# Optimization experiments

Hardware: AMD Instinct MI355X
Metric: run time of the kernel (lower is better)

## Reference

```python
import jax, jax.numpy as jnp
import numpy as np

EMBED_DIM = 1024
B, S = 4, 4096


def setup_inputs() -> dict:
    key = jax.random.key(0)
    kx, kq, kk, kv = jax.random.split(key, 4)
    x = jax.random.normal(kx, (B, S, EMBED_DIM), dtype=jnp.float32)
    W_Q = jax.random.normal(kq, (EMBED_DIM, EMBED_DIM), dtype=jnp.float32)
    W_K = jax.random.normal(kk, (EMBED_DIM, EMBED_DIM), dtype=jnp.float32)
    W_V = jax.random.normal(kv, (EMBED_DIM, EMBED_DIM), dtype=jnp.float32)
    return {"x": x, "W_Q": W_Q, "W_K": W_K, "W_V": W_V}


def reference(x, W_Q, W_K, W_V):
    # Q, K, V: [B, S, D]
    Q = x @ W_Q
    K = x @ W_K
    V = x @ W_V
    scale = 1.0 / jnp.sqrt(jnp.float32(EMBED_DIM))
    # scores: [B, S, S] (full score matrix, as in the original)
    scores = jnp.einsum('bsd,btd->bst', Q, K) * scale
    attn = jax.nn.softmax(scores, axis=-1)
    # output: [B, S, D]
    Z = jnp.einsum('bst,btd->bsd', attn, V)
    return Z
```

## Files before the change

kernel.cpp:

```cpp
#include <hip/hip_runtime.h>


typedef _Float16 half8 __attribute__((ext_vector_type(8)));
typedef _Float16 half4v __attribute__((ext_vector_type(4)));
typedef float floatx4 __attribute__((ext_vector_type(4)));

__device__ __forceinline__ void glds16(const _Float16* g, _Float16* l) {
    __builtin_amdgcn_global_load_lds(
        (const __attribute__((address_space(1))) void*)g,
        (__attribute__((address_space(3))) void*)l, 16, 0, 0);
}


struct QKTD { const _Float16* a; const _Float16* b; int ko; };

#define QK_VM(n) asm volatile("s_waitcnt vmcnt(" #n ")" ::: "memory")
#define QK_NOP ((void)0)

#define QK_PHASE(BUF, Q, STAGES, WAITS)                                         \
    do {                                                                        \
        if ((Q) == 0) {                                                         \
            _Pragma("unroll") for (int mi = 0; mi < 4; ++mi) {                  \
                af[mi][0] = *(const half8*)&sA[(BUF)*16384 + (abase + mi*16)*64 + s0]; \
                af[mi][1] = *(const half8*)&sA[(BUF)*16384 + (abase + mi*16)*64 + s1]; \
            }                                                                   \
        }                                                                       \
        half8 bf[2][2];                                                         \
        _Pragma("unroll") for (int nj = 0; nj < 2; ++nj) {                      \
            bf[nj][0] = *(const half8*)&sB[(BUF)*16384 + (bbase + (Q)*32 + nj*16)*64 + s0]; \
            bf[nj][1] = *(const half8*)&sB[(BUF)*16384 + (bbase + (Q)*32 + nj*16)*64 + s1]; \
        }                                                                       \
        STAGES;                                                                 \
        __builtin_amdgcn_sched_barrier(0);           \
        __builtin_amdgcn_s_barrier();                                           \
        asm volatile("s_waitcnt lgkmcnt(0)" ::: "memory");                      \
        __builtin_amdgcn_sched_barrier(0);                                      \
        __builtin_amdgcn_s_setprio(1);                                          \
        _Pragma("unroll") for (int mi = 0; mi < 4; ++mi)                        \
            _Pragma("unroll") for (int nj = 0; nj < 2; ++nj) {                  \
                acc[mi][(Q)*2 + nj] = __builtin_amdgcn_mfma_f32_16x16x32_f16(   \
                    af[mi][0], bf[nj][0], acc[mi][(Q)*2 + nj], 0, 0, 0);        \
                acc[mi][(Q)*2 + nj] = __builtin_amdgcn_mfma_f32_16x16x32_f16(   \
                    af[mi][1], bf[nj][1], acc[mi][(Q)*2 + nj], 0, 0, 0);        \
            }                                                                   \
        __builtin_amdgcn_s_setprio(0);                                          \
        WAITS;                                                                  \
        __builtin_amdgcn_s_barrier();                                           \
        __builtin_amdgcn_sched_barrier(0);                                      \
    } while (0)

__global__ __launch_bounds__(512, 2) void qk8(
    const _Float16* __restrict__ QH, const _Float16* __restrict__ QL,
    const _Float16* __restrict__ KH, const _Float16* __restrict__ KL,
    float* __restrict__ Sc, float* __restrict__ pmax, float scale)
{
    __shared__ _Float16 sA[2 * 256 * 64];
    __shared__ _Float16 sB[2 * 256 * 64];

    const int tid = threadIdx.x;
    const int bm = blockIdx.y, bn = blockIdx.x;
    const int lane = tid & 63, w = tid >> 6;
    const int quad = lane >> 4, lrow = lane & 15;
    const int wm = w >> 1, wn = w & 1;
    const int sx = lrow & 7;
    const int s0 = (quad ^ sx) * 8;
    const int s1 = s0 ^ 32;
    const int abase = wm * 64 + lrow;
    const int bbase = wn * 128 + lrow;
    const int wbase = w * 512;

    const int srow = tid >> 3;
    const int scol = ((tid & 7) ^ (srow & 7)) * 8;
    const size_t ga = (size_t)(bm * 256 + srow) * 1024 + scol;
    const size_t gb = (size_t)(bn * 256 + srow) * 1024 + scol;

    floatx4 acc[4][8] = {};
    half8 af[4][2];

    auto td = [&](int t) {
        const int d = t / 3, m = t - d * 3;
        return QKTD{m == 2 ? QL : QH, m == 1 ? KL : KH, d * 64};
    };
    auto stageA4 = [&](int b, QKTD s) {
        const _Float16* g = s.a + ga + s.ko;
        _Float16* l = sA + b * 16384 + wbase;
        glds16(g, l);
        glds16(g + 64 * 1024, l + 4096);
        glds16(g + 128 * 1024, l + 8192);
        glds16(g + 192 * 1024, l + 12288);
    };
    auto stageBq = [&](int b, int qr, QKTD s) {
        glds16(s.b + gb + (size_t)(qr * 64) * 1024 + s.ko,
               sB + b * 16384 + qr * 4096 + wbase);
    };

    {
        QKTD t0 = td(0), t1 = td(1);
        stageA4(0, t0);
        stageBq(0, 0, t0); stageBq(0, 2, t0);
        stageBq(0, 1, t0); stageBq(0, 3, t0);
        stageA4(1, t1);
        stageBq(1, 0, t1); stageBq(1, 2, t1);
    }
    __builtin_amdgcn_sched_barrier(0);
    QK_VM(6);
    __builtin_amdgcn_s_barrier();
    __builtin_amdgcn_sched_barrier(0);

    #pragma unroll 1
    for (int i = 0; i < 24; ++i) {
        const int i2 = 2 * i + 2 < 47 ? 2 * i + 2 : 47;
        const int i3 = 2 * i + 3 < 47 ? 2 * i + 3 : 47;
        const QKTD t1 = td(2 * i + 1);
        const QKTD ta = td(i2);
        const QKTD tb = td(i3);
        QK_PHASE(0, 0, { stageBq(1, 1, t1); stageBq(1, 3, t1); }, QK_NOP);
        QK_PHASE(0, 1, stageA4(0, ta), QK_VM(12));
        QK_PHASE(0, 2, { stageBq(0, 0, ta); stageBq(0, 2, ta); }, QK_NOP);
        QK_PHASE(0, 3, QK_NOP, QK_VM(8));
        QK_PHASE(1, 0, { stageBq(0, 1, ta); stageBq(0, 3, ta); }, QK_NOP);
        QK_PHASE(1, 1, stageA4(1, tb), QK_VM(12));
        QK_PHASE(1, 2, { stageBq(1, 0, tb); stageBq(1, 2, tb); }, QK_NOP);
        QK_PHASE(1, 3, QK_NOP, QK_VM(8));
    }

    QK_VM(0);
    __builtin_amdgcn_sched_barrier(0);

    #pragma unroll
    for (int mi = 0; mi < 4; ++mi) {
        #pragma unroll
        for (int r = 0; r < 4; ++r) {
            const int grow = bm * 256 + wm * 64 + mi * 16 + quad * 4 + r;
            float v[8];
            #pragma unroll
            for (int nc = 0; nc < 8; ++nc) v[nc] = acc[mi][nc][r] * scale;
            float mx = fmaxf(fmaxf(fmaxf(v[0], v[1]), fmaxf(v[2], v[3])),
                             fmaxf(fmaxf(v[4], v[5]), fmaxf(v[6], v[7])));
            #pragma unroll
            for (int off = 1; off < 16; off <<= 1)
                mx = fmaxf(mx, __shfl_xor(mx, off));
            if (lrow == 0) pmax[(size_t)grow * 32 + bn * 2 + wn] = mx;
            float* so = Sc + (size_t)grow * 4096 + bn * 256 + wn * 128;
            #pragma unroll
            for (int nc = 0; nc < 8; ++nc) so[nc * 16 + lrow] = v[nc];
        }
    }
}


template <bool SPLITIN, int OMODE, bool PMAX>
__global__ __launch_bounds__(256, 2) void gemm_nt(
    const _Float16* __restrict__ AH, const _Float16* __restrict__ AL,
    const _Float16* BH, const _Float16* BL,
    void* out0, void* out1,
    const float* __restrict__ rdiv, float* __restrict__ pmax,
    float scale, int M, int N, int K,
    const _Float16* BH2, const _Float16* BL2, void* o0b, void* o1b)
{
    if (blockIdx.z == 1) { BH = BH2; BL = BL2; out0 = o0b; out1 = o1b; }

    __shared__ _Float16 sAH[2 * 128 * 32];
    __shared__ _Float16 sBH[2 * 128 * 32];
    __shared__ _Float16 sAL[SPLITIN ? 2 * 128 * 32 : 8];
    __shared__ _Float16 sBL[SPLITIN ? 2 * 128 * 32 : 8];

    const int tid = threadIdx.x;
    const int bm = blockIdx.y, bn = blockIdx.x;
    const int lane = tid & 63, quad = lane >> 4, lrow = lane & 15;
    const int wave = tid >> 6, wm = wave >> 1, wn = wave & 1;

    const int wb = (tid & 192) * 8;
    const size_t g0 = (size_t)(tid >> 2) * K + (tid & 3) * 8;
    const size_t g1 = (size_t)((256 + tid) >> 2) * K + (tid & 3) * 8;
    const _Float16* pA0 = AH + (size_t)bm * 128 * K + g0;
    const _Float16* pA1 = AH + (size_t)bm * 128 * K + g1;
    const _Float16* pB0 = BH + (size_t)bn * 128 * K + g0;
    const _Float16* pB1 = BH + (size_t)bn * 128 * K + g1;
    const _Float16* pA0L = SPLITIN ? (AL + (size_t)bm * 128 * K + g0) : nullptr;
    const _Float16* pA1L = SPLITIN ? (AL + (size_t)bm * 128 * K + g1) : nullptr;
    const _Float16* pB0L = SPLITIN ? (BL + (size_t)bn * 128 * K + g0) : nullptr;
    const _Float16* pB1L = SPLITIN ? (BL + (size_t)bn * 128 * K + g1) : nullptr;

    floatx4 acc[4][4] = {};

    const int aoff = (wm * 64 + lrow) * 32 + quad * 8;
    const int boff = (wn * 64 + lrow) * 32 + quad * 8;

    glds16(pA0, sAH + wb);        glds16(pA1, sAH + 2048 + wb);
    glds16(pB0, sBH + wb);        glds16(pB1, sBH + 2048 + wb);
    if (SPLITIN) {
        glds16(pA0L, sAL + wb);   glds16(pA1L, sAL + 2048 + wb);
        glds16(pB0L, sBL + wb);   glds16(pB1L, sBL + 2048 + wb);
    }
    pA0 += 32; pA1 += 32; pB0 += 32; pB1 += 32;
    if (SPLITIN) { pA0L += 32; pA1L += 32; pB0L += 32; pB1L += 32; }

    int cur = 0;
    for (int k0 = 0; k0 < K; k0 += 32) {
        __syncthreads();

        if (k0 + 32 < K) {
            const int nb = (cur ^ 1) * 4096;
            glds16(pA0, sAH + nb + wb);        glds16(pA1, sAH + nb + 2048 + wb);
            glds16(pB0, sBH + nb + wb);        glds16(pB1, sBH + nb + 2048 + wb);
            if (SPLITIN) {
                glds16(pA0L, sAL + nb + wb);   glds16(pA1L, sAL + nb + 2048 + wb);
                glds16(pB0L, sBL + nb + wb);   glds16(pB1L, sBL + nb + 2048 + wb);
            }
            pA0 += 32; pA1 += 32; pB0 += 32; pB1 += 32;
            if (SPLITIN) { pA0L += 32; pA1L += 32; pB0L += 32; pB1L += 32; }
        }

        const int cb = cur * 4096;
        half8 aH[4], bH[4], aL[4], bL[4];
        #pragma unroll
        for (int i = 0; i < 4; ++i) {
            aH[i] = *(const half8*)&sAH[cb + aoff + i * 16 * 32];
            bH[i] = *(const half8*)&sBH[cb + boff + i * 16 * 32];
            if (SPLITIN) {
                aL[i] = *(const half8*)&sAL[cb + aoff + i * 16 * 32];
                bL[i] = *(const half8*)&sBL[cb + boff + i * 16 * 32];
            }
        }
        #pragma unroll
        for (int mi = 0; mi < 4; ++mi)
            #pragma unroll
            for (int nj = 0; nj < 4; ++nj) {
                acc[mi][nj] = __builtin_amdgcn_mfma_f32_16x16x32_f16(
                    aH[mi], bH[nj], acc[mi][nj], 0, 0, 0);
                if (SPLITIN) {
                    acc[mi][nj] = __builtin_amdgcn_mfma_f32_16x16x32_f16(
                        aH[mi], bL[nj], acc[mi][nj], 0, 0, 0);
                    acc[mi][nj] = __builtin_amdgcn_mfma_f32_16x16x32_f16(
                        aL[mi], bH[nj], acc[mi][nj], 0, 0, 0);
                }
            }
        cur ^= 1;
    }

    #pragma unroll
    for (int mi = 0; mi < 4; ++mi) {
        #pragma unroll
        for (int r = 0; r < 4; ++r) {
            const int grow = bm * 128 + wm * 64 + mi * 16 + quad * 4 + r;
            float s = scale;
            if (OMODE == 1) s = scale / rdiv[grow];
            float v[4];
            #pragma unroll
            for (int nj = 0; nj < 4; ++nj) v[nj] = acc[mi][nj][r] * s;
            if (PMAX) {
                float mx = fmaxf(fmaxf(v[0], v[1]), fmaxf(v[2], v[3]));
                #pragma unroll
                for (int off = 1; off < 16; off <<= 1)
                    mx = fmaxf(mx, __shfl_xor(mx, off));
                if (lrow == 0) pmax[(size_t)grow * 64 + bn * 2 + wn] = mx;
            }
            #pragma unroll
            for (int nj = 0; nj < 4; ++nj) {
                const int gcol = bn * 128 + wn * 64 + nj * 16 + lrow;
                const size_t idx = (size_t)grow * N + gcol;
                if (OMODE <= 1) {
                    ((float*)out0)[idx] = v[nj];
                } else if (OMODE == 2) {
                    ((_Float16*)out0)[idx] = (_Float16)v[nj];
                } else {
                    const _Float16 h = (_Float16)v[nj];
                    ((_Float16*)out0)[idx] = h;
                    ((_Float16*)out1)[idx] = (_Float16)(v[nj] - (float)h);
                }
            }
        }
    }
}

__global__ __launch_bounds__(256) void split_scale(
    const float* __restrict__ x, _Float16* __restrict__ hi,
    _Float16* __restrict__ lo, int n)
{
    int i = (blockIdx.x * 256 + threadIdx.x) * 4;
    const int stride = gridDim.x * 256 * 4;
    for (; i < n; i += stride) {
        float4 v = *(const float4*)(x + i);
        float a[4] = {v.x * 256.f, v.y * 256.f, v.z * 256.f, v.w * 256.f};
        half4v h, l;
        #pragma unroll
        for (int j = 0; j < 4; ++j) {
            h[j] = (_Float16)a[j];
            l[j] = (_Float16)(a[j] - (float)h[j]);
        }
        *(half4v*)(hi + i) = h;
        *(half4v*)(lo + i) = l;
    }
}

__global__ __launch_bounds__(256) void wprep3(
    const float* __restrict__ W0, const float* __restrict__ W1,
    const float* __restrict__ W2,
    _Float16* __restrict__ h0, _Float16* __restrict__ l0,
    _Float16* __restrict__ h1, _Float16* __restrict__ l1,
    _Float16* __restrict__ h2, int dim)
{
    const int z = blockIdx.z;
    const float* W = (z == 0) ? W0 : (z == 1) ? W1 : W2;
    _Float16* hiT = (z == 0) ? h0 : (z == 1) ? h1 : h2;
    _Float16* loT = (z == 0) ? l0 : (z == 1) ? l1 : nullptr;

    __shared__ float t[32][33];
    const int n0 = blockIdx.x * 32, k0 = blockIdx.y * 32;
    const int tx = threadIdx.x, ty = threadIdx.y;
    #pragma unroll
    for (int i = 0; i < 4; ++i)
        t[ty + 8 * i][tx] = 256.f * W[(size_t)(k0 + ty + 8 * i) * dim + n0 + tx];
    __syncthreads();
    #pragma unroll
    for (int i = 0; i < 4; ++i) {
        const int nn = ty + 8 * i;
        const float v = t[tx][nn];
        const _Float16 h = (_Float16)v;
        const size_t o = (size_t)(n0 + nn) * dim + k0 + tx;
        hiT[o] = h;
        if (loT) loT[o] = (_Float16)(v - (float)h);
    }
}

__global__ __launch_bounds__(256) void softmax_p(
    const float* __restrict__ Sc, const float* __restrict__ pmax,
    _Float16* __restrict__ P, float* __restrict__ rowsum)
{
    __shared__ float red[8];
    const int tid = threadIdx.x;
    const int row = blockIdx.x;
    const float* srow = Sc + (size_t)row * 4096;
    _Float16* prow = P + (size_t)row * 4096;

    if (tid < 32) {
        float m = pmax[(size_t)row * 32 + tid];
        #pragma unroll
        for (int off = 16; off; off >>= 1) m = fmaxf(m, __shfl_xor(m, off));
        if (tid == 0) red[0] = m;
    }
    __syncthreads();
    const float rmax = red[0];

    float s = 0.f;
    for (int c = tid * 4; c < 4096; c += 1024) {
        float4 v = *(const float4*)(srow + c);
        float p0 = __expf(v.x - rmax), p1 = __expf(v.y - rmax);
        float p2 = __expf(v.z - rmax), p3 = __expf(v.w - rmax);
        s += p0 + p1 + p2 + p3;
        half4v h = {(_Float16)p0, (_Float16)p1, (_Float16)p2, (_Float16)p3};
        *(half4v*)(prow + c) = h;
    }
    #pragma unroll
    for (int off = 32; off; off >>= 1) s += __shfl_xor(s, off, 64);
    if ((tid & 63) == 0) red[4 + (tid >> 6)] = s;
    __syncthreads();
    if (tid == 0) rowsum[row] = red[4] + red[5] + red[6] + red[7];
}

extern "C" void kernel_launch(void* const* d_in, const int* in_sizes, int n_in,
                              void* d_out, int out_size, void* d_ws, size_t ws_size,
                              hipStream_t stream) {
    const int Bb = 4, S = 4096, D = 1024;
    const size_t SD = (size_t)S * D;
    const size_t SS = (size_t)S * S;

    const float* x  = (const float*)d_in[0];
    const float* WQ = (const float*)d_in[1];
    const float* WK = (const float*)d_in[2];
    const float* WV = (const float*)d_in[3];
    float* out = (float*)d_out;

    char* w = (char*)d_ws;
    _Float16* WQhT = (_Float16*)w;  w += (size_t)D * D * 2;
    _Float16* WQlT = (_Float16*)w;  w += (size_t)D * D * 2;
    _Float16* WKhT = (_Float16*)w;  w += (size_t)D * D * 2;
    _Float16* WKlT = (_Float16*)w;  w += (size_t)D * D * 2;
    _Float16* WvhT = (_Float16*)w;  w += (size_t)D * D * 2;
    _Float16* xhi  = (_Float16*)w;  w += SD * 2;
    _Float16* xlo  = (_Float16*)w;  w += SD * 2;
    _Float16* Qhi  = (_Float16*)w;  w += SD * 2;
    _Float16* Qlo  = (_Float16*)w;  w += SD * 2;
    _Float16* Khi  = (_Float16*)w;  w += SD * 2;
    _Float16* Klo  = (_Float16*)w;  w += SD * 2;
    _Float16* VT   = (_Float16*)w;  w += SD * 2;
    float*    rowsum = (float*)w;   w += (size_t)S * 4;
    float*    pmax = (float*)w;     w += (size_t)S * 64 * 4;
    float*    Sc   = (float*)w;     w += SS * 4;
    _Float16* P    = (_Float16*)w;  w += SS * 2;

    const float kInv256 = 0.00390625f;
    const float kScScale = 4.76837158203125e-7f;

    dim3 blk(256);

    wprep3<<<dim3(32, 32, 3), dim3(32, 8), 0, stream>>>(
        WQ, WK, WV, WQhT, WQlT, WKhT, WKlT, WvhT, D);

    for (int b = 0; b < Bb; ++b) {
        const float* xb = x + (size_t)b * SD;
        float* outb = out + (size_t)b * SD;

        split_scale<<<dim3(4096), blk, 0, stream>>>(xb, xhi, xlo, (int)SD);

        gemm_nt<true, 3, false><<<dim3(D / 128, S / 128, 2), blk, 0, stream>>>(
            xhi, xlo, WQhT, WQlT, Qhi, Qlo, nullptr, nullptr, kInv256, S, D, D,
            WKhT, WKlT, Khi, Klo);

        gemm_nt<false, 2, false><<<dim3(S / 128, D / 128, 1), blk, 0, stream>>>(
            WvhT, nullptr, xhi, nullptr, VT, nullptr, nullptr, nullptr, kInv256,
            D, S, D, nullptr, nullptr, nullptr, nullptr);

        qk8<<<dim3(S / 256, S / 256), dim3(512), 0, stream>>>(
            Qhi, Qlo, Khi, Klo, Sc, pmax, kScScale);

        softmax_p<<<dim3(S), blk, 0, stream>>>(Sc, pmax, P, rowsum);

        gemm_nt<false, 1, false><<<dim3(D / 128, S / 128, 1), blk, 0, stream>>>(
            P, nullptr, VT, nullptr, outb, nullptr, rowsum, nullptr, kInv256,
            S, D, S, nullptr, nullptr, nullptr, nullptr);
    }
}
```

Before: 1.196 ms.

## Restructure QK GEMM pipeline to two barriers per K-tile with register double-buffered B

Replaces the eight-phase loop, which had two block barriers per quarter-tile, with a group schedule that software-pipelines LDS reads of B fragments into alternating register buffers so each MFMA batch overlaps the next fragment load. Global-to-LDS staging for a whole tile is issued at once after a single barrier, cutting the number of s_barrier syncs per tile from eight to two. This adds register pressure from the extra B fragment buffers and leaves less slack between staging and consumption.

```diff
diff --git a/kernel.cpp b/kernel.cpp
--- a/kernel.cpp
+++ b/kernel.cpp
@@ -15,38 +15,54 @@
 struct QKTD { const _Float16* a; const _Float16* b; int ko; };
 
 #define QK_VM(n) asm volatile("s_waitcnt vmcnt(" #n ")" ::: "memory")
-#define QK_NOP ((void)0)
-
-#define QK_PHASE(BUF, Q, STAGES, WAITS)                                         \
-    do {                                                                        \
-        if ((Q) == 0) {                                                         \
-            _Pragma("unroll") for (int mi = 0; mi < 4; ++mi) {                  \
-                af[mi][0] = *(const half8*)&sA[(BUF)*16384 + (abase + mi*16)*64 + s0]; \
-                af[mi][1] = *(const half8*)&sA[(BUF)*16384 + (abase + mi*16)*64 + s1]; \
-            }                                                                   \
-        }                                                                       \
-        half8 bf[2][2];                                                         \
-        _Pragma("unroll") for (int nj = 0; nj < 2; ++nj) {                      \
-            bf[nj][0] = *(const half8*)&sB[(BUF)*16384 + (bbase + (Q)*32 + nj*16)*64 + s0]; \
-            bf[nj][1] = *(const half8*)&sB[(BUF)*16384 + (bbase + (Q)*32 + nj*16)*64 + s1]; \
-        }                                                                       \
-        STAGES;                                                                 \
-        __builtin_amdgcn_sched_barrier(0);           \
-        __builtin_amdgcn_s_barrier();                                           \
-        asm volatile("s_waitcnt lgkmcnt(0)" ::: "memory");                      \
-        __builtin_amdgcn_sched_barrier(0);                                      \
-        __builtin_amdgcn_s_setprio(1);                                          \
-        _Pragma("unroll") for (int mi = 0; mi < 4; ++mi)                        \
-            _Pragma("unroll") for (int nj = 0; nj < 2; ++nj) {                  \
-                acc[mi][(Q)*2 + nj] = __builtin_amdgcn_mfma_f32_16x16x32_f16(   \
-                    af[mi][0], bf[nj][0], acc[mi][(Q)*2 + nj], 0, 0, 0);        \
-                acc[mi][(Q)*2 + nj] = __builtin_amdgcn_mfma_f32_16x16x32_f16(   \
-                    af[mi][1], bf[nj][1], acc[mi][(Q)*2 + nj], 0, 0, 0);        \
-            }                                                                   \
-        __builtin_amdgcn_s_setprio(0);                                          \
-        WAITS;                                                                  \
-        __builtin_amdgcn_s_barrier();                                           \
-        __builtin_amdgcn_sched_barrier(0);                                      \
+#define QK_FENCE asm volatile("" ::: "memory")
+#define QK_BAR                                                                 \
+    do { QK_FENCE; __builtin_amdgcn_s_barrier(); QK_FENCE;                     \
+         __builtin_amdgcn_sched_barrier(0); } while (0)
+
+#define QK_LDA(BUF)                                                            \
+    do { _Pragma("unroll") for (int mi = 0; mi < 4; ++mi) {                    \
+        af[mi][0] = *(const half8*)&sA[(BUF)*16384 + (abase + mi*16)*64 + s0]; \
+        af[mi][1] = *(const half8*)&sA[(BUF)*16384 + (abase + mi*16)*64 + s1]; \
+    } __builtin_amdgcn_sched_barrier(0); } while (0)
+
+#define QK_LDB(BUF, Q, DST)                                                    \
+    do { _Pragma("unroll") for (int nj = 0; nj < 2; ++nj) {                    \
+        DST[nj][0] = *(const half8*)&sB[(BUF)*16384 + (bbase + (Q)*32 + nj*16)*64 + s0]; \
+        DST[nj][1] = *(const half8*)&sB[(BUF)*16384 + (bbase + (Q)*32 + nj*16)*64 + s1]; \
+    } __builtin_amdgcn_sched_barrier(0); } while (0)
+
+#define QK_MFMA(Q, BF)                                                         \
+    do { __builtin_amdgcn_s_setprio(1);                                        \
+    _Pragma("unroll") for (int mi = 0; mi < 4; ++mi)                           \
+        _Pragma("unroll") for (int nj = 0; nj < 2; ++nj) {                     \
+            acc[mi][(Q)*2 + nj] = __builtin_amdgcn_mfma_f32_16x16x32_f16(      \
+                af[mi][0], BF[nj][0], acc[mi][(Q)*2 + nj], 0, 0, 0);           \
+            acc[mi][(Q)*2 + nj] = __builtin_amdgcn_mfma_f32_16x16x32_f16(      \
+                af[mi][1], BF[nj][1], acc[mi][(Q)*2 + nj], 0, 0, 0);           \
+        }                                                                      \
+    __builtin_amdgcn_s_setprio(0);                                             \
+    __builtin_amdgcn_sched_barrier(0); } while (0)
+
+#define QK_GROUP(BUF, TS)                                                      \
+    do {                                                                       \
+        QK_LDA(BUF);                                                           \
+        QK_LDB(BUF, 1, bfB);                                                   \
+        QK_MFMA(0, bfA);                                                       \
+        QK_LDB(BUF, 2, bfA);                                                   \
+        QK_MFMA(1, bfB);                                                       \
+        QK_LDB(BUF, 3, bfB);                                                   \
+        QK_MFMA(2, bfA);                                                       \
+        asm volatile("s_waitcnt lgkmcnt(0)" ::: "memory");                     \
+        QK_BAR;                                                                \
+        stageA4(BUF, TS);                                                      \
+        stageBq(BUF, 0, TS); stageBq(BUF, 1, TS);                              \
+        stageBq(BUF, 2, TS); stageBq(BUF, 3, TS);                              \
+        __builtin_amdgcn_sched_barrier(0);                                     \
+        QK_VM(8);                                                              \
+        QK_BAR;                                                                \
+        QK_LDB((BUF) ^ 1, 0, bfA);                                             \
+        QK_MFMA(3, bfB);                                                       \
     } while (0)
 
 __global__ __launch_bounds__(512, 2) void qk8(
@@ -75,7 +91,7 @@
     const size_t gb = (size_t)(bn * 256 + srow) * 1024 + scol;
 
     floatx4 acc[4][8] = {};
-    half8 af[4][2];
+    half8 af[4][2], bfA[2][2], bfB[2][2];
 
     auto td = [&](int t) {
         const int d = t / 3, m = t - d * 3;
@@ -97,34 +113,29 @@
     {
         QKTD t0 = td(0), t1 = td(1);
         stageA4(0, t0);
-        stageBq(0, 0, t0); stageBq(0, 2, t0);
-        stageBq(0, 1, t0); stageBq(0, 3, t0);
+        stageBq(0, 0, t0); stageBq(0, 1, t0);
+        stageBq(0, 2, t0); stageBq(0, 3, t0);
         stageA4(1, t1);
-        stageBq(1, 0, t1); stageBq(1, 2, t1);
+        stageBq(1, 0, t1); stageBq(1, 1, t1);
+        stageBq(1, 2, t1); stageBq(1, 3, t1);
     }
     __builtin_amdgcn_sched_barrier(0);
-    QK_VM(6);
-    __builtin_amdgcn_s_barrier();
-    __builtin_amdgcn_sched_barrier(0);
+    QK_VM(8);
+    QK_BAR;
+    QK_LDB(0, 0, bfA);
 
     #pragma unroll 1
     for (int i = 0; i < 24; ++i) {
         const int i2 = 2 * i + 2 < 47 ? 2 * i + 2 : 47;
         const int i3 = 2 * i + 3 < 47 ? 2 * i + 3 : 47;
-        const QKTD t1 = td(2 * i + 1);
         const QKTD ta = td(i2);
         const QKTD tb = td(i3);
-        QK_PHASE(0, 0, { stageBq(1, 1, t1); stageBq(1, 3, t1); }, QK_NOP);
-        QK_PHASE(0, 1, stageA4(0, ta), QK_VM(12));
-        QK_PHASE(0, 2, { stageBq(0, 0, ta); stageBq(0, 2, ta); }, QK_NOP);
-        QK_PHASE(0, 3, QK_NOP, QK_VM(8));
-        QK_PHASE(1, 0, { stageBq(0, 1, ta); stageBq(0, 3, ta); }, QK_NOP);
-        QK_PHASE(1, 1, stageA4(1, tb), QK_VM(12));
-        QK_PHASE(1, 2, { stageBq(1, 0, tb); stageBq(1, 2, tb); }, QK_NOP);
-        QK_PHASE(1, 3, QK_NOP, QK_VM(8));
+        QK_GROUP(0, ta);
+        QK_GROUP(1, tb);
     }
 
     QK_VM(0);
+    asm volatile("s_waitcnt lgkmcnt(0)" ::: "memory");
     __builtin_amdgcn_sched_barrier(0);
 
     #pragma unroll
```

Result: no change. 1.204 ms (+0.6%).
